# Optimization experiments

Measured on AMD Instinct MI355X. Metric: run time of the kernel, lower is better.

The kernel has to match this reference:

```python
import jax, jax.numpy as jnp
import numpy as np

B, H1, W1 = 2, 64, 96        # batch, 1/8-res grid
H2, W2 = 64, 96              # cost-map spatial dims
HEADS = 1                    # cfg.cost_heads_num
R = 4                        # lookup radius -> 9x9 window


def setup_inputs() -> dict:
    key = jax.random.key(0)
    k1, k2, k3, k4 = jax.random.split(key, 4)
    N = B * H1 * W1
    cost_maps = jax.random.normal(k1, (N, HEADS, H2, W2), jnp.float32)
    # coords1 in pixel space of the (H2, W2) map: channel 0 = x, channel 1 = y
    scale = jnp.array([W2 - 1.0, H2 - 1.0], jnp.float32)[None, :, None, None]
    coords = jax.random.uniform(k2, (B, 2, H1, W1), jnp.float32) * scale
    flow = jax.random.normal(k3, (B, 2, H1, W1), jnp.float32) * 2.0
    mask = jax.random.normal(k4, (B, 64 * 9, H1, W1), jnp.float32)
    return {"cost_maps": cost_maps, "coords": coords, "flow": flow, "mask": mask}


def bilinear_sampler(img, coords):
    """grid_sample(align_corners=True, padding_mode='zeros') in pixel coords.
    img: [N, C, H, W]; coords: [N, P, Q, 2] with last dim (x, y)."""
    N, C, H, W = img.shape
    P = coords.shape[1] * coords.shape[2]
    x = coords[..., 0].reshape(N, P)
    y = coords[..., 1].reshape(N, P)
    x0 = jnp.floor(x); y0 = jnp.floor(y)
    wx = x - x0; wy = y - y0
    imgf = img.reshape(N, C, H * W)

    def gather(xi, yi):
        valid = ((xi >= 0) & (xi <= W - 1) & (yi >= 0) & (yi <= H - 1)).astype(img.dtype)
        xc = jnp.clip(xi, 0, W - 1).astype(jnp.int32)
        yc = jnp.clip(yi, 0, H - 1).astype(jnp.int32)
        idx = yc * W + xc                                   # [N, P]
        v = jnp.take_along_axis(imgf, jnp.broadcast_to(idx[:, None, :], (N, C, P)), axis=2)
        return v * valid[:, None, :]

    out = (gather(x0, y0) * ((1 - wx) * (1 - wy))[:, None, :]
           + gather(x0 + 1, y0) * (wx * (1 - wy))[:, None, :]
           + gather(x0, y0 + 1) * ((1 - wx) * wy)[:, None, :]
           + gather(x0 + 1, y0 + 1) * (wx * wy)[:, None, :])
    return out.reshape(N, C, coords.shape[1], coords.shape[2])


def encode_flow_token(cost_maps, coords):
    """cost_maps: [B*H1*W1, heads, H2, W2]; coords: [B, 2, H1, W1] -> [B, heads*81, H1, W1]"""
    b, _, h1, w1 = coords.shape
    c = coords.transpose(0, 2, 3, 1)                        # [B, H1, W1, 2]
    d = jnp.linspace(-R, R, 2 * R + 1, dtype=coords.dtype)
    gy, gx = jnp.meshgrid(d, d, indexing="ij")
    delta = jnp.stack([gy, gx], axis=-1)[None]               # [1, 9, 9, 2]
    centroid = c.reshape(b * h1 * w1, 1, 1, 2)
    lookup = centroid + delta                                # [BHW, 9, 9, 2] (x, y)
    corr = bilinear_sampler(cost_maps, lookup)               # [BHW, heads, 9, 9]
    corr = corr.reshape(b, h1, w1, -1).transpose(0, 3, 1, 2)
    return corr


def upsample_flow(flow, mask):
    """Convex upsample [N,2,H,W] -> [N,2,8H,8W]."""
    N, _, H, W = flow.shape
    m = jax.nn.softmax(mask.reshape(N, 1, 9, 8, 8, H, W), axis=2)
    fp = jnp.pad(8.0 * flow, ((0, 0), (0, 0), (1, 1), (1, 1)))
    # F.unfold(3x3): kernel positions row-major, channel-major layout
    patches = jnp.stack([fp[:, :, i:i + H, j:j + W] for i in range(3) for j in range(3)], axis=2)
    up = jnp.sum(m * patches[:, :, :, None, None, :, :], axis=2)   # [N, 2, 8, 8, H, W]
    up = up.transpose(0, 1, 4, 2, 5, 3)                            # [N, 2, H, 8, W, 8]
    return up.reshape(N, 2, 8 * H, 8 * W)


def reference(cost_maps, coords, flow, mask):
    corr = encode_flow_token(cost_maps, coords)
    up_flow = upsample_flow(flow, mask)
    return (corr, up_flow)
```

## Files before the change

kernel.cpp:

```cpp
#include <hip/hip_runtime.h>

#define B_    2
#define H1_   64
#define W1_   96
#define H2_   64
#define W2_   96
#define HW_   (H1_ * W1_)
#define KWIN  81
#define CORR_ELEMS (B_ * KWIN * HW_)
#define UP_HW      (8 * H1_ * 8 * W1_)

#define CORR_PIX    (B_ * HW_)
#define CORR_BLOCKS (CORR_PIX / 64)
#define UP_THREADS  (B_ * H1_ * 8 * W1_)
#define UP_BLOCKS   (UP_THREADS / 256)
#define TOT_BLOCKS  (CORR_BLOCKS + UP_BLOCKS)

#define PSTRIDE 101

__global__ __launch_bounds__(256) void fused_kernel(const float* __restrict__ cost,
                                                    const float* __restrict__ coords,
                                                    const float* __restrict__ flow,
                                                    const float* __restrict__ mask,
                                                    float* __restrict__ out) {
    __shared__ float patch[64 * PSTRIDE];
    __shared__ int   xi0s[64];
    __shared__ int   yi0s[64];

    if (blockIdx.x < CORR_BLOCKS) {
        int tid  = threadIdx.x;
        int lane = tid & 63;
        int g    = tid >> 6;
        int m    = blockIdx.x * 64 + lane;
        int b    = m / HW_;
        int rem  = m - b * HW_;

        float cx = coords[b * 2 * HW_ + rem];
        float cy = coords[b * 2 * HW_ + HW_ + rem];
        float xf = floorf(cx), yf = floorf(cy);
        float wx = cx - xf,   wy = cy - yf;
        int xi0 = (int)xf - 4;
        int yi0 = (int)yf - 4;
        float w00 = (1.0f - wx) * (1.0f - wy);
        float w10 = wx * (1.0f - wy);
        float w01 = (1.0f - wx) * wy;
        float w11 = wx * wy;

        if (tid < 64) { xi0s[tid] = xi0; yi0s[tid] = yi0; }
        __syncthreads();

        const float* __restrict__ cmB = cost + (size_t)blockIdx.x * 64 * HW_;
#pragma unroll
        for (int it = 0; it < 25; ++it) {
            unsigned l  = it * 256u + tid;
            unsigned px = l / 100u;
            unsigned e  = l - px * 100u;
            unsigned r  = e / 10u;
            unsigned c  = e - r * 10u;
            int y = yi0s[px] + (int)r;
            int x = xi0s[px] + (int)c;
            bool ok = (x >= 0) & (x < W2_) & (y >= 0) & (y < H2_);
            int yc = min(max(y, 0), H2_ - 1);
            int xc = min(max(x, 0), W2_ - 1);
            float v = cmB[px * HW_ + yc * W2_ + xc];
            patch[px * PSTRIDE + e] = ok ? v : 0.0f;
        }
        __syncthreads();

        const float* __restrict__ pp = patch + lane * PSTRIDE;
        size_t obase = (size_t)b * KWIN * HW_ + rem;
        int start = (g == 0) ? 0 : (1 + 20 * g);
        int count = (g == 0) ? 21 : 20;
        for (int t = 0; t < count; ++t) {
            int ch = start + t;
            int p  = ch / 9;
            int q  = ch - p * 9;
            int o  = q * 10 + p;
            float val = w00 * pp[o]      + w10 * pp[o + 1]
                      + w01 * pp[o + 10] + w11 * pp[o + 11];
            out[obase + (size_t)ch * HW_] = val;
        }
    } else {
        int t = (blockIdx.x - CORR_BLOCKS) * 256 + threadIdx.x;
        int w = t % W1_;
        int u = t / W1_;
        int r = u % 8; u /= 8;
        int h = u % H1_;
        int n = u / H1_;

        const float* __restrict__ mp = mask + ((size_t)n * 576 + r * 8) * HW_ + h * W1_ + w;
        float mv[9][8];
#pragma unroll
        for (int k = 0; k < 9; ++k)
#pragma unroll
            for (int s = 0; s < 8; ++s)
                mv[k][s] = mp[(size_t)(k * 64 + s) * HW_];

        float scale[8];
#pragma unroll
        for (int s = 0; s < 8; ++s) {
            float mx = mv[0][s];
#pragma unroll
            for (int k = 1; k < 9; ++k) mx = fmaxf(mx, mv[k][s]);
            float sum = 0.0f;
#pragma unroll
            for (int k = 0; k < 9; ++k) { mv[k][s] = __expf(mv[k][s] - mx); sum += mv[k][s]; }
            scale[s] = 8.0f / sum;
        }

        const float* __restrict__ f0p = flow + (size_t)n * 2 * HW_;
        const float* __restrict__ f1p = f0p + HW_;
        float a0[8], a1[8];
#pragma unroll
        for (int s = 0; s < 8; ++s) { a0[s] = 0.0f; a1[s] = 0.0f; }

#pragma unroll
        for (int di = 0; di < 3; ++di) {
#pragma unroll
            for (int dj = 0; dj < 3; ++dj) {
                int k = di * 3 + dj;
                int hh = h + di - 1, ww = w + dj - 1;
                bool ok = (hh >= 0) & (hh < H1_) & (ww >= 0) & (ww < W1_);
                float fv0 = ok ? f0p[hh * W1_ + ww] : 0.0f;
                float fv1 = ok ? f1p[hh * W1_ + ww] : 0.0f;
#pragma unroll
                for (int s = 0; s < 8; ++s) {
                    a0[s] += mv[k][s] * fv0;
                    a1[s] += mv[k][s] * fv1;
                }
            }
        }

        float* outU = out + CORR_ELEMS;
        size_t ob = ((size_t)(n * 2 + 0) * (8 * H1_) + h * 8 + r) * (8 * W1_) + (size_t)w * 8;
        float4 c0a = make_float4(a0[0] * scale[0], a0[1] * scale[1], a0[2] * scale[2], a0[3] * scale[3]);
        float4 c0b = make_float4(a0[4] * scale[4], a0[5] * scale[5], a0[6] * scale[6], a0[7] * scale[7]);
        float4 c1a = make_float4(a1[0] * scale[0], a1[1] * scale[1], a1[2] * scale[2], a1[3] * scale[3]);
        float4 c1b = make_float4(a1[4] * scale[4], a1[5] * scale[5], a1[6] * scale[6], a1[7] * scale[7]);
        *(float4*)(outU + ob)              = c0a;
        *(float4*)(outU + ob + 4)          = c0b;
        *(float4*)(outU + ob + UP_HW)      = c1a;
        *(float4*)(outU + ob + UP_HW + 4)  = c1b;
    }
}

extern "C" void kernel_launch(void* const* d_in, const int* in_sizes, int n_in,
                              void* d_out, int out_size, void* d_ws, size_t ws_size,
                              hipStream_t stream) {
    const float* cost   = (const float*)d_in[0];
    const float* coords = (const float*)d_in[1];
    const float* flow   = (const float*)d_in[2];
    const float* mask   = (const float*)d_in[3];
    float* out = (float*)d_out;

    fused_kernel<<<TOT_BLOCKS, 256, 0, stream>>>(cost, coords, flow, mask, out);
}
```

Baseline: 16.47 us.

## Halve per-block work and interleave correlation and upsample blocks

Correlation blocks now handle 32 pixels instead of 64, and upsample threads compute 4 subpixels instead of 8, doubling the block counts. Blocks alternate roles with a 1:2 modulo pattern so both workloads spread evenly over the CUs. Fewer registers per upsample thread should raise occupancy. In exchange, flow neighbors are loaded redundantly and there are more blocks to schedule.

New measurement: 17.12 us. 1.04x slower.

```diff
diff --git a/kernel.cpp b/kernel.cpp
--- a/kernel.cpp
+++ b/kernel.cpp
@@ -11,8 +11,8 @@
 #define UP_HW      (8 * H1_ * 8 * W1_)
 
 #define CORR_PIX    (B_ * HW_)
-#define CORR_BLOCKS (CORR_PIX / 64)
-#define UP_THREADS  (B_ * H1_ * 8 * W1_)
+#define CORR_BLOCKS (CORR_PIX / 32)
+#define UP_THREADS  (B_ * H1_ * 8 * 2 * W1_)
 #define UP_BLOCKS   (UP_THREADS / 256)
 #define TOT_BLOCKS  (CORR_BLOCKS + UP_BLOCKS)
 
@@ -23,15 +23,16 @@
                                                     const float* __restrict__ flow,
                                                     const float* __restrict__ mask,
                                                     float* __restrict__ out) {
-    __shared__ float patch[64 * PSTRIDE];
-    __shared__ int   xi0s[64];
-    __shared__ int   yi0s[64];
+    __shared__ float patch[32 * PSTRIDE];
+    __shared__ int   xi0s[32];
+    __shared__ int   yi0s[32];
 
-    if (blockIdx.x < CORR_BLOCKS) {
+    int role = blockIdx.x % 3;
+    if (role == 0) {
+        int cid  = blockIdx.x / 3;
         int tid  = threadIdx.x;
-        int lane = tid & 63;
-        int g    = tid >> 6;
-        int m    = blockIdx.x * 64 + lane;
+        int px   = tid & 31;
+        int m    = cid * 32 + px;
         int b    = m / HW_;
         int rem  = m - b * HW_;
 
@@ -46,73 +47,82 @@
         float w01 = (1.0f - wx) * wy;
         float w11 = wx * wy;
 
-        if (tid < 64) { xi0s[tid] = xi0; yi0s[tid] = yi0; }
+        if (tid < 32) { xi0s[tid] = xi0; yi0s[tid] = yi0; }
         __syncthreads();
 
-        const float* __restrict__ cmB = cost + (size_t)blockIdx.x * 64 * HW_;
+        const float* __restrict__ cmB = cost + (size_t)(cid * 32) * HW_;
 #pragma unroll
-        for (int it = 0; it < 25; ++it) {
-            unsigned l  = it * 256u + tid;
-            unsigned px = l / 100u;
-            unsigned e  = l - px * 100u;
-            unsigned r  = e / 10u;
-            unsigned c  = e - r * 10u;
-            int y = yi0s[px] + (int)r;
-            int x = xi0s[px] + (int)c;
-            bool ok = (x >= 0) & (x < W2_) & (y >= 0) & (y < H2_);
-            int yc = min(max(y, 0), H2_ - 1);
-            int xc = min(max(x, 0), W2_ - 1);
-            float v = cmB[px * HW_ + yc * W2_ + xc];
-            patch[px * PSTRIDE + e] = ok ? v : 0.0f;
+        for (int it = 0; it < 13; ++it) {
+            int l = it * 256 + tid;
+            if (l < 3200) {
+                unsigned pl = (unsigned)l / 100u;
+                unsigned e  = (unsigned)l - pl * 100u;
+                unsigned r  = e / 10u;
+                unsigned c  = e - r * 10u;
+                int y = yi0s[pl] + (int)r;
+                int x = xi0s[pl] + (int)c;
+                bool ok = (x >= 0) & (x < W2_) & (y >= 0) & (y < H2_);
+                int yc = min(max(y, 0), H2_ - 1);
+                int xc = min(max(x, 0), W2_ - 1);
+                float v = cmB[pl * HW_ + yc * W2_ + xc];
+                patch[pl * PSTRIDE + e] = ok ? v : 0.0f;
+            }
         }
         __syncthreads();
 
-        const float* __restrict__ pp = patch + lane * PSTRIDE;
+        const float* __restrict__ pp = patch + px * PSTRIDE;
         size_t obase = (size_t)b * KWIN * HW_ + rem;
-        int start = (g == 0) ? 0 : (1 + 20 * g);
-        int count = (g == 0) ? 21 : 20;
-        for (int t = 0; t < count; ++t) {
-            int ch = start + t;
-            int p  = ch / 9;
-            int q  = ch - p * 9;
-            int o  = q * 10 + p;
-            float val = w00 * pp[o]      + w10 * pp[o + 1]
-                      + w01 * pp[o + 10] + w11 * pp[o + 11];
-            out[obase + (size_t)ch * HW_] = val;
+        int g = tid >> 5;
+#pragma unroll
+        for (int t = 0; t < 11; ++t) {
+            int ch = g + 8 * t;
+            if (ch < KWIN) {
+                int p = ch / 9;
+                int q = ch - p * 9;
+                int o = q * 10 + p;
+                float val = w00 * pp[o]      + w10 * pp[o + 1]
+                          + w01 * pp[o + 10] + w11 * pp[o + 11];
+                out[obase + (size_t)ch * HW_] = val;
+            }
         }
     } else {
-        int t = (blockIdx.x - CORR_BLOCKS) * 256 + threadIdx.x;
-        int w = t % W1_;
-        int u = t / W1_;
-        int r = u % 8; u /= 8;
-        int h = u % H1_;
-        int n = u / H1_;
+        int uid = blockIdx.x - blockIdx.x / 3 - 1;
+        int t = uid * 256 + threadIdx.x;
+        int w  = t % W1_;
+        int t2 = t / W1_;
+        int sh = t2 & 1;
+        int t3 = t2 >> 1;
+        int r  = t3 & 7;
+        int t4 = t3 >> 3;
+        int h  = t4 & 63;
+        int n  = t4 >> 6;
 
-        const float* __restrict__ mp = mask + ((size_t)n * 576 + r * 8) * HW_ + h * W1_ + w;
-        float mv[9][8];
+        const float* __restrict__ mp =
+            mask + ((size_t)n * 576 + r * 8 + sh * 4) * HW_ + h * W1_ + w;
+        float mv[9][4];
 #pragma unroll
         for (int k = 0; k < 9; ++k)
 #pragma unroll
-            for (int s = 0; s < 8; ++s)
-                mv[k][s] = mp[(size_t)(k * 64 + s) * HW_];
+            for (int j = 0; j < 4; ++j)
+                mv[k][j] = mp[(size_t)(k * 64 + j) * HW_];
 
-        float scale[8];
+        float scale[4];
 #pragma unroll
-        for (int s = 0; s < 8; ++s) {
-            float mx = mv[0][s];
+        for (int j = 0; j < 4; ++j) {
+            float mx = mv[0][j];
 #pragma unroll
-            for (int k = 1; k < 9; ++k) mx = fmaxf(mx, mv[k][s]);
+            for (int k = 1; k < 9; ++k) mx = fmaxf(mx, mv[k][j]);
             float sum = 0.0f;
 #pragma unroll
-            for (int k = 0; k < 9; ++k) { mv[k][s] = __expf(mv[k][s] - mx); sum += mv[k][s]; }
-            scale[s] = 8.0f / sum;
+            for (int k = 0; k < 9; ++k) { mv[k][j] = __expf(mv[k][j] - mx); sum += mv[k][j]; }
+            scale[j] = 8.0f / sum;
         }
 
         const float* __restrict__ f0p = flow + (size_t)n * 2 * HW_;
         const float* __restrict__ f1p = f0p + HW_;
-        float a0[8], a1[8];
+        float a0[4], a1[4];
 #pragma unroll
-        for (int s = 0; s < 8; ++s) { a0[s] = 0.0f; a1[s] = 0.0f; }
+        for (int j = 0; j < 4; ++j) { a0[j] = 0.0f; a1[j] = 0.0f; }
 
 #pragma unroll
         for (int di = 0; di < 3; ++di) {
@@ -124,23 +134,22 @@
                 float fv0 = ok ? f0p[hh * W1_ + ww] : 0.0f;
                 float fv1 = ok ? f1p[hh * W1_ + ww] : 0.0f;
 #pragma unroll
-                for (int s = 0; s < 8; ++s) {
-                    a0[s] += mv[k][s] * fv0;
-                    a1[s] += mv[k][s] * fv1;
+                for (int j = 0; j < 4; ++j) {
+                    a0[j] += mv[k][j] * fv0;
+                    a1[j] += mv[k][j] * fv1;
                 }
             }
         }
 
         float* outU = out + CORR_ELEMS;
-        size_t ob = ((size_t)(n * 2 + 0) * (8 * H1_) + h * 8 + r) * (8 * W1_) + (size_t)w * 8;
-        float4 c0a = make_float4(a0[0] * scale[0], a0[1] * scale[1], a0[2] * scale[2], a0[3] * scale[3]);
-        float4 c0b = make_float4(a0[4] * scale[4], a0[5] * scale[5], a0[6] * scale[6], a0[7] * scale[7]);
-        float4 c1a = make_float4(a1[0] * scale[0], a1[1] * scale[1], a1[2] * scale[2], a1[3] * scale[3]);
-        float4 c1b = make_float4(a1[4] * scale[4], a1[5] * scale[5], a1[6] * scale[6], a1[7] * scale[7]);
-        *(float4*)(outU + ob)              = c0a;
-        *(float4*)(outU + ob + 4)          = c0b;
-        *(float4*)(outU + ob + UP_HW)      = c1a;
-        *(float4*)(outU + ob + UP_HW + 4)  = c1b;
+        size_t ob = ((size_t)(n * 2 + 0) * (8 * H1_) + h * 8 + r) * (8 * W1_)
+                  + (size_t)w * 8 + sh * 4;
+        float4 c0 = make_float4(a0[0] * scale[0], a0[1] * scale[1],
+                                a0[2] * scale[2], a0[3] * scale[3]);
+        float4 c1 = make_float4(a1[0] * scale[0], a1[1] * scale[1],
+                                a1[2] * scale[2], a1[3] * scale[3]);
+        *(float4*)(outU + ob)         = c0;
+        *(float4*)(outU + ob + UP_HW) = c1;
     }
 }
 
```
